# Kernel optimization log

Measured on AMD Instinct MI355X. Metric: run time of the kernel, lower is better.

## Reference

```python
import jax, jax.numpy as jnp
import numpy as np

N = 20000      # nodes
E = 640000     # edges
F = 128        # input features
H = 256        # hidden dim
G = 64         # graphs in batch


def setup_inputs() -> dict:
    key = jax.random.key(0)
    ks = jax.random.split(key, 24)
    w = lambda k, sh: (jax.random.normal(k, sh, jnp.float32) * 0.05)
    inp = {
        'x': jax.random.normal(ks[0], (N, F), jnp.float32),
        'edge_index': jax.random.randint(ks[1], (2, E), 0, N, dtype=jnp.int32),
        'batch': jnp.sort(jax.random.randint(ks[2], (N,), 0, G, dtype=jnp.int32)),
        # GCN stack
        'gcn_w1': w(ks[3], (F, H)), 'gcn_b1': jnp.zeros((H,), jnp.float32),
        'gcn_w2': w(ks[4], (H, H)), 'gcn_b2': jnp.zeros((H,), jnp.float32),
        'gcn_w3': w(ks[5], (H, H)), 'gcn_b3': jnp.zeros((H,), jnp.float32),
        'gcn_w4': w(ks[6], (H, H)), 'gcn_b4': jnp.zeros((H,), jnp.float32),
        # EdgeConv 1: Linear(2F,H) -> ReLU -> Linear(H,H)
        'ec1_w1': w(ks[7], (2 * F, H)), 'ec1_b1': jnp.zeros((H,), jnp.float32),
        'ec1_w2': w(ks[8], (H, H)),     'ec1_b2': jnp.zeros((H,), jnp.float32),
        # EdgeConv 2: Linear(2H,H) -> ReLU -> Linear(H,H)
        'ec2_w1': w(ks[9], (2 * H, H)), 'ec2_b1': jnp.zeros((H,), jnp.float32),
        'ec2_w2': w(ks[10], (H, H)),    'ec2_b2': jnp.zeros((H,), jnp.float32),
        # head
        'fc1_w': w(ks[11], (2 * H, H)), 'fc1_b': jnp.zeros((H,), jnp.float32),
        'out_w': w(ks[12], (H, 1)),     'out_b': jnp.zeros((1,), jnp.float32),
    }
    return inp


def _gcn_conv(x, W, b, src, dst, n):
    # PyG GCNConv: add self loops, symmetric deg^-1/2 normalization, scatter-sum.
    h = x @ W                                        # [n, H]
    loops = jnp.arange(n, dtype=src.dtype)
    s = jnp.concatenate([src, loops])
    d = jnp.concatenate([dst, loops])
    deg = jax.ops.segment_sum(jnp.ones(s.shape[0], x.dtype), d, num_segments=n)
    dinv = jnp.where(deg > 0, jax.lax.rsqrt(deg), 0.0)
    norm = (dinv[s] * dinv[d])[:, None]              # [E+n, 1]
    return jax.ops.segment_sum(h[s] * norm, d, num_segments=n) + b


def _edge_conv(x, w1, b1, w2, b2, src, dst, n):
    # PyG EdgeConv: msg = MLP([x_i, x_j - x_i]), max-aggregate at target i.
    xi = x[dst]
    xj = x[src]
    m = jnp.concatenate([xi, xj - xi], axis=1)       # [E, 2*d]
    m = jax.nn.relu(m @ w1 + b1) @ w2 + b2           # [E, H]
    out = jax.ops.segment_max(m, dst, num_segments=n)
    return jnp.where(jnp.isfinite(out), out, 0.0)    # empty segments -> 0


def reference(x, edge_index, batch,
              gcn_w1, gcn_b1, gcn_w2, gcn_b2, gcn_w3, gcn_b3, gcn_w4, gcn_b4,
              ec1_w1, ec1_b1, ec1_w2, ec1_b2, ec2_w1, ec2_b1, ec2_w2, ec2_b2,
              fc1_w, fc1_b, out_w, out_b):
    n = x.shape[0]
    src, dst = edge_index[0], edge_index[1]
    relu = jax.nn.relu
    # GCN branch (dropout is identity at inference)
    xg = relu(_gcn_conv(x, gcn_w1, gcn_b1, src, dst, n))
    xg = relu(_gcn_conv(xg, gcn_w2, gcn_b2, src, dst, n))
    xg = relu(_gcn_conv(xg, gcn_w3, gcn_b3, src, dst, n))
    xg = relu(_gcn_conv(xg, gcn_w4, gcn_b4, src, dst, n))
    # EdgeConv branch
    xe = relu(_edge_conv(x, ec1_w1, ec1_b1, ec1_w2, ec1_b2, src, dst, n))
    xe = relu(_edge_conv(xe, ec2_w1, ec2_b1, ec2_w2, ec2_b2, src, dst, n))
    # pool per graph + head
    x_cat = jnp.concatenate([xg, xe], axis=1)        # [n, 512]
    g = jax.ops.segment_sum(x_cat, batch, num_segments=G)  # [G, 512]
    g = relu(g @ fc1_w + fc1_b)
    return g @ out_w + out_b                          # [G, 1]
```

## Files before the change

### kernel.cpp

```cpp
#include <hip/hip_runtime.h>

#define HD 256

typedef __attribute__((ext_vector_type(8))) __bf16 bf16x8;
typedef __attribute__((ext_vector_type(4))) __bf16 bf16x4;
typedef __attribute__((ext_vector_type(4))) float f32x4;

static __device__ __forceinline__ float relu_f(float x){ return x > 0.f ? x : 0.f; }

static __device__ __forceinline__ void split4(const float* m, bf16x4& vh, bf16x4& vl){
    #pragma unroll
    for (int j = 0; j < 4; j++){
        float v = m[j];
        __bf16 h = (__bf16)v;
        vh[j] = h;
        vl[j] = (__bf16)(v - (float)h);
    }
}

__global__ void k_count(const int* __restrict__ dst, int* __restrict__ cnt, int E){
    int i = blockIdx.x * blockDim.x + threadIdx.x;
    if (i < E) atomicAdd(&cnt[dst[i]], 1);
}

__global__ void k_dinv(const int* __restrict__ cnt, float* __restrict__ dinv, int n){
    int i = blockIdx.x * blockDim.x + threadIdx.x;
    if (i < n) dinv[i] = 1.0f / sqrtf((float)(cnt[i] + 1));
}

__global__ void k_scan(const int* __restrict__ cnt, int* __restrict__ row_ptr, int n){
    __shared__ int lds[1024];
    int t = threadIdx.x;
    int carry = 0;
    for (int base = 0; base < n; base += 1024){
        int idx = base + t;
        int v = (idx < n) ? cnt[idx] : 0;
        __syncthreads();
        lds[t] = v;
        __syncthreads();
        for (int off = 1; off < 1024; off <<= 1){
            int add = (t >= off) ? lds[t - off] : 0;
            __syncthreads();
            lds[t] += add;
            __syncthreads();
        }
        int incl = lds[t];
        if (idx < n) row_ptr[idx] = carry + incl - v;
        carry += lds[1023];
    }
    if (t == 0) row_ptr[n] = carry;
}

__global__ void k_fill(const int* __restrict__ src, const int* __restrict__ dst,
                       const int* __restrict__ row_ptr, int* __restrict__ fill,
                       int* __restrict__ csr_src, int* __restrict__ csr_dst, int E){
    int i = blockIdx.x * blockDim.x + threadIdx.x;
    if (i < E){
        int d = dst[i];
        int pos = row_ptr[d] + atomicAdd(&fill[d], 1);
        csr_src[pos] = src[i];
        csr_dst[pos] = d;
    }
}

struct PackDesc { const float* src; const float* src2; __bf16* ph; __bf16* pl; int K; int pad; };
struct PackArgs { PackDesc d[10]; };

__global__ void k_wpack_all(PackArgs a){
    PackDesc p = a.d[blockIdx.y];
    int total = (p.K >> 5) * 8192;
    int idx = blockIdx.x * 256 + threadIdx.x;
    if (idx >= total) return;
    int j = idx & 7, g = (idx >> 3) & 3, c = (idx >> 5) & 255, ks = idx >> 13;
    int k = ks * 32 + g * 8 + j;
    float v = p.src[(size_t)k * HD + c];
    if (p.src2) v -= p.src2[(size_t)k * HD + c];
    __bf16 h = (__bf16)v;
    p.ph[idx] = h;
    p.pl[idx] = (__bf16)(v - (float)h);
}

__global__ __launch_bounds__(512, 4) void k_gemm_mfma(
    const float* __restrict__ A,
    const __bf16* __restrict__ Wph, const __bf16* __restrict__ Wpl,
    const float* __restrict__ bias,
    float* __restrict__ C, int M, int K)
{
    __shared__ __bf16 mh[2][64][40];
    __shared__ __bf16 ml[2][64][40];
    int t = threadIdx.x;
    int m0 = blockIdx.x * 64;
    const int w = t >> 6, fr = t & 15, fg = (t & 63) >> 4;
    const int srow = t >> 3, skb = (t & 7) * 4;
    int ar = m0 + srow; if (ar >= M) ar = M - 1;
    const float* Arow = A + (size_t)ar * K + skb;
    const int c0 = w * 32 + fr;
    const int KS = K >> 5;

    f32x4 acc[4][2];
    #pragma unroll
    for (int i = 0; i < 4; i++)
        #pragma unroll
        for (int j = 0; j < 2; j++) acc[i][j] = (f32x4){0.f, 0.f, 0.f, 0.f};

    {
        float4 av = *(const float4*)(Arow);
        float m4[4] = {av.x, av.y, av.z, av.w};
        bf16x4 vh, vl;
        split4(m4, vh, vl);
        *(bf16x4*)&mh[0][srow][skb] = vh;
        *(bf16x4*)&ml[0][srow][skb] = vl;
    }

    for (int ks = 0; ks < KS; ++ks){
        float4 av;
        if (ks + 1 < KS) av = *(const float4*)(Arow + (ks + 1) * 32);
        bf16x8 bh[2], bl[2];
        #pragma unroll
        for (int nf = 0; nf < 2; nf++){
            size_t bi = ((size_t)(ks * 256 + c0 + nf * 16) * 4 + fg) * 8;
            bh[nf] = *(const bf16x8*)(Wph + bi);
            bl[nf] = *(const bf16x8*)(Wpl + bi);
        }
        __syncthreads();
        const int cb = ks & 1;
        #pragma unroll
        for (int mf = 0; mf < 4; mf++){
            bf16x8 ah = *(const bf16x8*)&mh[cb][mf * 16 + fr][fg * 8];
            bf16x8 al = *(const bf16x8*)&ml[cb][mf * 16 + fr][fg * 8];
            #pragma unroll
            for (int nf = 0; nf < 2; nf++){
                acc[mf][nf] = __builtin_amdgcn_mfma_f32_16x16x32_bf16(ah, bh[nf], acc[mf][nf], 0, 0, 0);
                acc[mf][nf] = __builtin_amdgcn_mfma_f32_16x16x32_bf16(al, bh[nf], acc[mf][nf], 0, 0, 0);
                acc[mf][nf] = __builtin_amdgcn_mfma_f32_16x16x32_bf16(ah, bl[nf], acc[mf][nf], 0, 0, 0);
            }
        }
        if (ks + 1 < KS){
            float m4[4] = {av.x, av.y, av.z, av.w};
            bf16x4 vh, vl;
            split4(m4, vh, vl);
            *(bf16x4*)&mh[cb ^ 1][srow][skb] = vh;
            *(bf16x4*)&ml[cb ^ 1][srow][skb] = vl;
        }
    }

    float bj[2];
    #pragma unroll
    for (int nf = 0; nf < 2; nf++) bj[nf] = bias ? bias[c0 + nf * 16] : 0.f;
    #pragma unroll
    for (int mf = 0; mf < 4; mf++)
        #pragma unroll
        for (int reg = 0; reg < 4; reg++){
            int row = m0 + mf * 16 + fg * 4 + reg;
            if (row < M){
                #pragma unroll
                for (int nf = 0; nf < 2; nf++)
                    C[(size_t)row * HD + c0 + nf * 16] = acc[mf][nf][reg] + bj[nf];
            }
        }
}

__global__ __launch_bounds__(256) void k_gcn_agg(const float* __restrict__ h,
                                                 const float* __restrict__ dinv,
                                                 const int* __restrict__ row_ptr,
                                                 const int* __restrict__ csr_src,
                                                 const float* __restrict__ bias,
                                                 float* __restrict__ out, int n){
    int wid = threadIdx.x >> 6, lane = threadIdx.x & 63;
    int i = blockIdx.x * 4 + wid;
    if (i >= n) return;
    float di = dinv[i];
    const float4* hp = (const float4*)h;
    float4 v = hp[(size_t)i * 64 + lane];
    float ax = v.x * di, ay = v.y * di, az = v.z * di, aw = v.w * di;
    int e0 = row_ptr[i], e1 = row_ptr[i + 1];
    for (int e = e0; e < e1; e++){
        int s = csr_src[e];
        float ds = dinv[s];
        float4 u = hp[(size_t)s * 64 + lane];
        ax += u.x * ds; ay += u.y * ds; az += u.z * ds; aw += u.w * ds;
    }
    const float4 b = ((const float4*)bias)[lane];
    float4 o;
    o.x = relu_f(ax * di + b.x);
    o.y = relu_f(ay * di + b.y);
    o.z = relu_f(az * di + b.z);
    o.w = relu_f(aw * di + b.w);
    ((float4*)out)[(size_t)i * 64 + lane] = o;
}

__global__ __launch_bounds__(512, 4) void k_edge_mfma(
    const float* __restrict__ A, const float* __restrict__ B,
    const __bf16* __restrict__ Wph, const __bf16* __restrict__ Wpl,
    const float* __restrict__ bias,
    const int* __restrict__ csr_src, const int* __restrict__ csr_dst,
    float* __restrict__ out, int E)
{
    __shared__ __bf16 mh[2][64][40];
    __shared__ __bf16 ml[2][64][40];
    __shared__ int sdst[64], ssrc[64];
    int t = threadIdx.x;
    int nwg = gridDim.x;
    int q = nwg >> 3, r = nwg & 7;
    int xc = blockIdx.x & 7;
    int bid = (xc < r ? xc * (q + 1) : r * (q + 1) + (xc - r) * q) + (blockIdx.x >> 3);
    int p0 = bid * 64;
    if (t < 64){
        int e = p0 + t; if (e >= E) e = E - 1;
        sdst[t] = csr_dst[e];
        ssrc[t] = csr_src[e];
    }
    __syncthreads();

    const int w  = t >> 6;
    const int fr = t & 15;
    const int fg = (t & 63) >> 4;
    const int srow = t >> 3, skb = (t & 7) * 4;
    const float* Arow = A + (size_t)sdst[srow] * HD + skb;
    const float* Brow = B + (size_t)ssrc[srow] * HD + skb;
    const int c0 = w * 32 + fr;

    f32x4 acc[4][2];
    #pragma unroll
    for (int i = 0; i < 4; i++)
        #pragma unroll
        for (int j = 0; j < 2; j++) acc[i][j] = (f32x4){0.f, 0.f, 0.f, 0.f};

    {
        float4 a = *(const float4*)(Arow);
        float4 g = *(const float4*)(Brow);
        float m4[4] = {relu_f(a.x + g.x), relu_f(a.y + g.y), relu_f(a.z + g.z), relu_f(a.w + g.w)};
        bf16x4 vh, vl;
        split4(m4, vh, vl);
        *(bf16x4*)&mh[0][srow][skb] = vh;
        *(bf16x4*)&ml[0][srow][skb] = vl;
    }

    for (int ks = 0; ks < 8; ++ks){
        float4 a, g;
        if (ks < 7){
            a = *(const float4*)(Arow + (ks + 1) * 32);
            g = *(const float4*)(Brow + (ks + 1) * 32);
        }
        bf16x8 bh[2], bl[2];
        #pragma unroll
        for (int nf = 0; nf < 2; nf++){
            size_t bi = ((size_t)(ks * 256 + c0 + nf * 16) * 4 + fg) * 8;
            bh[nf] = *(const bf16x8*)(Wph + bi);
            bl[nf] = *(const bf16x8*)(Wpl + bi);
        }
        __syncthreads();
        const int cb = ks & 1;
        #pragma unroll
        for (int mf = 0; mf < 4; mf++){
            bf16x8 ah = *(const bf16x8*)&mh[cb][mf * 16 + fr][fg * 8];
            bf16x8 al = *(const bf16x8*)&ml[cb][mf * 16 + fr][fg * 8];
            #pragma unroll
            for (int nf = 0; nf < 2; nf++){
                acc[mf][nf] = __builtin_amdgcn_mfma_f32_16x16x32_bf16(ah, bh[nf], acc[mf][nf], 0, 0, 0);
                acc[mf][nf] = __builtin_amdgcn_mfma_f32_16x16x32_bf16(al, bh[nf], acc[mf][nf], 0, 0, 0);
                acc[mf][nf] = __builtin_amdgcn_mfma_f32_16x16x32_bf16(ah, bl[nf], acc[mf][nf], 0, 0, 0);
            }
        }
        if (ks < 7){
            float m4[4] = {relu_f(a.x + g.x), relu_f(a.y + g.y), relu_f(a.z + g.z), relu_f(a.w + g.w)};
            bf16x4 vh, vl;
            split4(m4, vh, vl);
            *(bf16x4*)&mh[cb ^ 1][srow][skb] = vh;
            *(bf16x4*)&ml[cb ^ 1][srow][skb] = vl;
        }
    }

    float bj[2];
    #pragma unroll
    for (int nf = 0; nf < 2; nf++) bj[nf] = bias[c0 + nf * 16];
    int curd = sdst[fg * 4];
    float v[2];
    #pragma unroll
    for (int nf = 0; nf < 2; nf++) v[nf] = acc[0][nf][0] + bj[nf];
    #pragma unroll
    for (int mf = 0; mf < 4; mf++){
        #pragma unroll
        for (int reg = 0; reg < 4; reg++){
            if (mf == 0 && reg == 0) continue;
            int d = sdst[mf * 16 + fg * 4 + reg];
            if (d != curd){
                #pragma unroll
                for (int nf = 0; nf < 2; nf++)
                    if (v[nf] > 0.f)
                        atomicMax((int*)(out + (size_t)curd * HD + c0 + nf * 16), __float_as_int(v[nf]));
                curd = d;
                #pragma unroll
                for (int nf = 0; nf < 2; nf++) v[nf] = acc[mf][nf][reg] + bj[nf];
            } else {
                #pragma unroll
                for (int nf = 0; nf < 2; nf++) v[nf] = fmaxf(v[nf], acc[mf][nf][reg] + bj[nf]);
            }
        }
    }
    #pragma unroll
    for (int nf = 0; nf < 2; nf++)
        if (v[nf] > 0.f)
            atomicMax((int*)(out + (size_t)curd * HD + c0 + nf * 16), __float_as_int(v[nf]));
}

__global__ __launch_bounds__(512) void k_pool(const float* __restrict__ xg,
                                              const float* __restrict__ xe,
                                              const int* __restrict__ batch,
                                              float* __restrict__ gpool, int n){
    int g = blockIdx.x, t = threadIdx.x;
    int lo, hi;
    { int l = 0, h = n; while (l < h){ int m = (l + h) >> 1; if (batch[m] < g) l = m + 1; else h = m; } lo = l; }
    { int l = lo, h = n; while (l < h){ int m = (l + h) >> 1; if (batch[m] < g + 1) l = m + 1; else h = m; } hi = l; }
    const float* sp = (t < 256) ? (xg + t) : (xe + (t - 256));
    float a0 = 0.f, a1 = 0.f;
    int i = lo;
    for (; i + 1 < hi; i += 2){
        a0 += sp[(size_t)i * HD];
        a1 += sp[(size_t)(i + 1) * HD];
    }
    if (i < hi) a0 += sp[(size_t)i * HD];
    gpool[g * 512 + t] = a0 + a1;
}

__global__ __launch_bounds__(256) void k_head(const float* __restrict__ gpool,
                                              const float* __restrict__ w1,
                                              const float* __restrict__ b1,
                                              const float* __restrict__ w2,
                                              const float* __restrict__ b2,
                                              float* __restrict__ out){
    __shared__ float red[256];
    int g = blockIdx.x, t = threadIdx.x;
    float acc = b1[t];
    const float* gp = gpool + g * 512;
    #pragma unroll 4
    for (int k = 0; k < 512; k++) acc += gp[k] * w1[k * HD + t];
    red[t] = relu_f(acc) * w2[t];
    __syncthreads();
    for (int s = 128; s > 0; s >>= 1){
        if (t < s) red[t] += red[t + s];
        __syncthreads();
    }
    if (t == 0) out[g] = red[0] + b2[0];
}

extern "C" void kernel_launch(void* const* d_in, const int* in_sizes, int n_in,
                              void* d_out, int out_size, void* d_ws, size_t ws_size,
                              hipStream_t stream){
    const float* x      = (const float*)d_in[0];
    const int*   ei     = (const int*)d_in[1];
    const int*   batch  = (const int*)d_in[2];
    const float* gcn_w[4] = {(const float*)d_in[3], (const float*)d_in[5], (const float*)d_in[7], (const float*)d_in[9]};
    const float* gcn_b[4] = {(const float*)d_in[4], (const float*)d_in[6], (const float*)d_in[8], (const float*)d_in[10]};
    const float* ec1_w1 = (const float*)d_in[11]; const float* ec1_b1 = (const float*)d_in[12];
    const float* ec1_w2 = (const float*)d_in[13]; const float* ec1_b2 = (const float*)d_in[14];
    const float* ec2_w1 = (const float*)d_in[15]; const float* ec2_b1 = (const float*)d_in[16];
    const float* ec2_w2 = (const float*)d_in[17]; const float* ec2_b2 = (const float*)d_in[18];
    const float* fc1_w  = (const float*)d_in[19]; const float* fc1_b  = (const float*)d_in[20];
    const float* out_w  = (const float*)d_in[21]; const float* out_b  = (const float*)d_in[22];

    const int N = in_sizes[2];
    const int E = in_sizes[1] / 2;
    const int F = in_sizes[0] / N;
    const int* src = ei;
    const int* dst = ei + E;
    const int GB64 = (N + 63) / 64;
    const int EB   = (E + 63) / 64;

    char* w = (char*)d_ws;
    auto alloc = [&](size_t bytes) -> char* {
        char* p = w;
        w += (bytes + 255) & ~(size_t)255;
        return p;
    };
    int*   cnt     = (int*)alloc((size_t)N * 4);
    int*   fillc   = (int*)alloc((size_t)N * 4);
    int*   row_ptr = (int*)alloc((size_t)(N + 1) * 4);
    int*   csr_src = (int*)alloc((size_t)E * 4);
    int*   csr_dst = (int*)alloc((size_t)E * 4);
    float* dinv    = (float*)alloc((size_t)N * 4);
    float* act     = (float*)alloc((size_t)N * HD * 4);
    float* hbuf    = (float*)alloc((size_t)N * HD * 4);
    float* Bbuf    = (float*)alloc((size_t)N * HD * 4);
    float* xebuf   = (float*)alloc((size_t)N * HD * 4);
    float* gpool   = (float*)alloc((size_t)64 * 512 * 4);
    auto packa = [&](int K) -> __bf16* { return (__bf16*)alloc((size_t)K * 256 * 2); };
    __bf16* pg1h = packa(128); __bf16* pg1l = packa(128);
    __bf16* pg2h = packa(256); __bf16* pg2l = packa(256);
    __bf16* pg3h = packa(256); __bf16* pg3l = packa(256);
    __bf16* pg4h = packa(256); __bf16* pg4l = packa(256);
    __bf16* pe1ah = packa(128); __bf16* pe1al = packa(128);
    __bf16* pe1bh = packa(128); __bf16* pe1bl = packa(128);
    __bf16* pe2ah = packa(256); __bf16* pe2al = packa(256);
    __bf16* pe2bh = packa(256); __bf16* pe2bl = packa(256);
    __bf16* w2h1 = packa(256); __bf16* w2l1 = packa(256);
    __bf16* w2h2 = packa(256); __bf16* w2l2 = packa(256);

    hipMemsetAsync(cnt, 0, (size_t)N * 4, stream);
    hipMemsetAsync(fillc, 0, (size_t)N * 4, stream);
    k_count<<<(E + 255) / 256, 256, 0, stream>>>(dst, cnt, E);
    k_dinv<<<(N + 255) / 256, 256, 0, stream>>>(cnt, dinv, N);
    k_scan<<<1, 1024, 0, stream>>>(cnt, row_ptr, N);
    k_fill<<<(E + 255) / 256, 256, 0, stream>>>(src, dst, row_ptr, fillc, csr_src, csr_dst, E);

    PackArgs pa;
    pa.d[0] = {gcn_w[0],                  nullptr,                    pg1h,  pg1l,  F,  0};
    pa.d[1] = {gcn_w[1],                  nullptr,                    pg2h,  pg2l,  HD, 0};
    pa.d[2] = {gcn_w[2],                  nullptr,                    pg3h,  pg3l,  HD, 0};
    pa.d[3] = {gcn_w[3],                  nullptr,                    pg4h,  pg4l,  HD, 0};
    pa.d[4] = {ec1_w1,                    ec1_w1 + (size_t)F * HD,    pe1ah, pe1al, F,  0};
    pa.d[5] = {ec1_w1 + (size_t)F * HD,   nullptr,                    pe1bh, pe1bl, F,  0};
    pa.d[6] = {ec2_w1,                    ec2_w1 + (size_t)HD * HD,   pe2ah, pe2al, HD, 0};
    pa.d[7] = {ec2_w1 + (size_t)HD * HD,  nullptr,                    pe2bh, pe2bl, HD, 0};
    pa.d[8] = {ec1_w2,                    nullptr,                    w2h1,  w2l1,  HD, 0};
    pa.d[9] = {ec2_w2,                    nullptr,                    w2h2,  w2l2,  HD, 0};
    k_wpack_all<<<dim3(256, 10), 256, 0, stream>>>(pa);

    k_gemm_mfma<<<GB64, 512, 0, stream>>>(x, pg1h, pg1l, nullptr, hbuf, N, F);
    k_gcn_agg<<<(N + 3) / 4, 256, 0, stream>>>(hbuf, dinv, row_ptr, csr_src, gcn_b[0], act, N);
    const __bf16* pgh[3] = {pg2h, pg3h, pg4h};
    const __bf16* pgl[3] = {pg2l, pg3l, pg4l};
    for (int l = 0; l < 3; l++){
        k_gemm_mfma<<<GB64, 512, 0, stream>>>(act, pgh[l], pgl[l], nullptr, hbuf, N, HD);
        k_gcn_agg<<<(N + 3) / 4, 256, 0, stream>>>(hbuf, dinv, row_ptr, csr_src, gcn_b[l + 1], act, N);
    }

    k_gemm_mfma<<<GB64, 512, 0, stream>>>(x, pe1ah, pe1al, ec1_b1, hbuf, N, F);
    k_gemm_mfma<<<GB64, 512, 0, stream>>>(x, pe1bh, pe1bl, nullptr, Bbuf, N, F);
    hipMemsetAsync(xebuf, 0, (size_t)N * HD * 4, stream);
    k_edge_mfma<<<EB, 512, 0, stream>>>(hbuf, Bbuf, w2h1, w2l1, ec1_b2, csr_src, csr_dst, xebuf, E);

    k_gemm_mfma<<<GB64, 512, 0, stream>>>(xebuf, pe2ah, pe2al, ec2_b1, hbuf, N, HD);
    k_gemm_mfma<<<GB64, 512, 0, stream>>>(xebuf, pe2bh, pe2bl, nullptr, Bbuf, N, HD);
    hipMemsetAsync(xebuf, 0, (size_t)N * HD * 4, stream);
    k_edge_mfma<<<EB, 512, 0, stream>>>(hbuf, Bbuf, w2h2, w2l2, ec2_b2, csr_src, csr_dst, xebuf, E);

    k_pool<<<64, 512, 0, stream>>>(act, xebuf, batch, gpool, N);
    k_head<<<64, 256, 0, stream>>>(gpool, fc1_w, fc1_b, out_w, out_b, (float*)d_out);
}
```

Measured before the change: 1.332 ms.

## Prefetch A rows into registers, unroll GCN gather, fuse small kernels

The GEMM is templated on K-steps and now loads all of a thread's A chunks into registers up front. The edge kernel prefetches its gathered rows four steps ahead, hiding global latency behind the MFMA work. The GCN aggregation loop is unrolled by four with independent accumulators so more neighbour gathers are in flight at once. The dinv computation is folded into the scan kernel, and pooling plus the head are fused into one kernel, which removes launches. These changes raise register pressure under the 512x4 launch bounds, and the reordered fp32 sums change rounding slightly.

```diff
diff --git a/kernel.cpp b/kernel.cpp
--- a/kernel.cpp
+++ b/kernel.cpp
@@ -23,18 +23,15 @@
     if (i < E) atomicAdd(&cnt[dst[i]], 1);
 }
 
-__global__ void k_dinv(const int* __restrict__ cnt, float* __restrict__ dinv, int n){
-    int i = blockIdx.x * blockDim.x + threadIdx.x;
-    if (i < n) dinv[i] = 1.0f / sqrtf((float)(cnt[i] + 1));
-}
-
-__global__ void k_scan(const int* __restrict__ cnt, int* __restrict__ row_ptr, int n){
+__global__ void k_scan(const int* __restrict__ cnt, int* __restrict__ row_ptr,
+                       float* __restrict__ dinv, int n){
     __shared__ int lds[1024];
     int t = threadIdx.x;
     int carry = 0;
     for (int base = 0; base < n; base += 1024){
         int idx = base + t;
         int v = (idx < n) ? cnt[idx] : 0;
+        if (idx < n) dinv[idx] = 1.0f / sqrtf((float)(v + 1));
         __syncthreads();
         lds[t] = v;
         __syncthreads();
@@ -80,6 +77,7 @@
     p.pl[idx] = (__bf16)(v - (float)h);
 }
 
+template<int KS>
 __global__ __launch_bounds__(512, 4) void k_gemm_mfma(
     const float* __restrict__ A,
     const __bf16* __restrict__ Wph, const __bf16* __restrict__ Wpl,
@@ -95,26 +93,29 @@
     int ar = m0 + srow; if (ar >= M) ar = M - 1;
     const float* Arow = A + (size_t)ar * K + skb;
     const int c0 = w * 32 + fr;
-    const int KS = K >> 5;
-
-    f32x4 acc[4][2];
-    #pragma unroll
-    for (int i = 0; i < 4; i++)
-        #pragma unroll
-        for (int j = 0; j < 2; j++) acc[i][j] = (f32x4){0.f, 0.f, 0.f, 0.f};
-
-    {
-        float4 av = *(const float4*)(Arow);
-        float m4[4] = {av.x, av.y, av.z, av.w};
+
+    auto stage = [&](int buf, const float4& a){
+        float m4[4] = {a.x, a.y, a.z, a.w};
         bf16x4 vh, vl;
         split4(m4, vh, vl);
-        *(bf16x4*)&mh[0][srow][skb] = vh;
-        *(bf16x4*)&ml[0][srow][skb] = vl;
-    }
-
+        *(bf16x4*)&mh[buf][srow][skb] = vh;
+        *(bf16x4*)&ml[buf][srow][skb] = vl;
+    };
+
+    f32x4 acc[4][2];
+    #pragma unroll
+    for (int i = 0; i < 4; i++)
+        #pragma unroll
+        for (int j = 0; j < 2; j++) acc[i][j] = (f32x4){0.f, 0.f, 0.f, 0.f};
+
+    float4 rA[KS];
+    #pragma unroll
+    for (int c = 0; c < KS; c++) rA[c] = *(const float4*)(Arow + c * 32);
+
+    stage(0, rA[0]);
+
+    #pragma unroll
     for (int ks = 0; ks < KS; ++ks){
-        float4 av;
-        if (ks + 1 < KS) av = *(const float4*)(Arow + (ks + 1) * 32);
         bf16x8 bh[2], bl[2];
         #pragma unroll
         for (int nf = 0; nf < 2; nf++){
@@ -135,13 +136,7 @@
                 acc[mf][nf] = __builtin_amdgcn_mfma_f32_16x16x32_bf16(ah, bl[nf], acc[mf][nf], 0, 0, 0);
             }
         }
-        if (ks + 1 < KS){
-            float m4[4] = {av.x, av.y, av.z, av.w};
-            bf16x4 vh, vl;
-            split4(m4, vh, vl);
-            *(bf16x4*)&mh[cb ^ 1][srow][skb] = vh;
-            *(bf16x4*)&ml[cb ^ 1][srow][skb] = vl;
-        }
+        if (ks + 1 < KS) stage(cb ^ 1, rA[ks + 1]);
     }
 
     float bj[2];
@@ -172,14 +167,34 @@
     float di = dinv[i];
     const float4* hp = (const float4*)h;
     float4 v = hp[(size_t)i * 64 + lane];
-    float ax = v.x * di, ay = v.y * di, az = v.z * di, aw = v.w * di;
+    float ax0 = v.x * di, ay0 = v.y * di, az0 = v.z * di, aw0 = v.w * di;
+    float ax1 = 0.f, ay1 = 0.f, az1 = 0.f, aw1 = 0.f;
+    float ax2 = 0.f, ay2 = 0.f, az2 = 0.f, aw2 = 0.f;
+    float ax3 = 0.f, ay3 = 0.f, az3 = 0.f, aw3 = 0.f;
     int e0 = row_ptr[i], e1 = row_ptr[i + 1];
-    for (int e = e0; e < e1; e++){
+    int e = e0;
+    for (; e + 3 < e1; e += 4){
+        int s0 = csr_src[e], s1 = csr_src[e + 1], s2 = csr_src[e + 2], s3 = csr_src[e + 3];
+        float q0 = dinv[s0], q1 = dinv[s1], q2 = dinv[s2], q3 = dinv[s3];
+        float4 u0 = hp[(size_t)s0 * 64 + lane];
+        float4 u1 = hp[(size_t)s1 * 64 + lane];
+        float4 u2 = hp[(size_t)s2 * 64 + lane];
+        float4 u3 = hp[(size_t)s3 * 64 + lane];
+        ax0 += u0.x * q0; ay0 += u0.y * q0; az0 += u0.z * q0; aw0 += u0.w * q0;
+        ax1 += u1.x * q1; ay1 += u1.y * q1; az1 += u1.z * q1; aw1 += u1.w * q1;
+        ax2 += u2.x * q2; ay2 += u2.y * q2; az2 += u2.z * q2; aw2 += u2.w * q2;
+        ax3 += u3.x * q3; ay3 += u3.y * q3; az3 += u3.z * q3; aw3 += u3.w * q3;
+    }
+    for (; e < e1; e++){
         int s = csr_src[e];
-        float ds = dinv[s];
+        float q = dinv[s];
         float4 u = hp[(size_t)s * 64 + lane];
-        ax += u.x * ds; ay += u.y * ds; az += u.z * ds; aw += u.w * ds;
-    }
+        ax0 += u.x * q; ay0 += u.y * q; az0 += u.z * q; aw0 += u.w * q;
+    }
+    float ax = (ax0 + ax1) + (ax2 + ax3);
+    float ay = (ay0 + ay1) + (ay2 + ay3);
+    float az = (az0 + az1) + (az2 + az3);
+    float aw = (aw0 + aw1) + (aw2 + aw3);
     const float4 b = ((const float4*)bias)[lane];
     float4 o;
     o.x = relu_f(ax * di + b.x);
@@ -220,27 +235,33 @@
     const float* Brow = B + (size_t)ssrc[srow] * HD + skb;
     const int c0 = w * 32 + fr;
 
-    f32x4 acc[4][2];
-    #pragma unroll
-    for (int i = 0; i < 4; i++)
-        #pragma unroll
-        for (int j = 0; j < 2; j++) acc[i][j] = (f32x4){0.f, 0.f, 0.f, 0.f};
-
-    {
-        float4 a = *(const float4*)(Arow);
-        float4 g = *(const float4*)(Brow);
+    auto stage = [&](int buf, const float4& a, const float4& g){
         float m4[4] = {relu_f(a.x + g.x), relu_f(a.y + g.y), relu_f(a.z + g.z), relu_f(a.w + g.w)};
         bf16x4 vh, vl;
         split4(m4, vh, vl);
-        *(bf16x4*)&mh[0][srow][skb] = vh;
-        *(bf16x4*)&ml[0][srow][skb] = vl;
-    }
-
+        *(bf16x4*)&mh[buf][srow][skb] = vh;
+        *(bf16x4*)&ml[buf][srow][skb] = vl;
+    };
+
+    f32x4 acc[4][2];
+    #pragma unroll
+    for (int i = 0; i < 4; i++)
+        #pragma unroll
+        for (int j = 0; j < 2; j++) acc[i][j] = (f32x4){0.f, 0.f, 0.f, 0.f};
+
+    float4 ra[4], rg[4];
+    #pragma unroll
+    for (int c = 0; c < 4; c++){
+        ra[c] = *(const float4*)(Arow + c * 32);
+        rg[c] = *(const float4*)(Brow + c * 32);
+    }
+    stage(0, ra[0], rg[0]);
+
+    #pragma unroll
     for (int ks = 0; ks < 8; ++ks){
-        float4 a, g;
-        if (ks < 7){
-            a = *(const float4*)(Arow + (ks + 1) * 32);
-            g = *(const float4*)(Brow + (ks + 1) * 32);
+        if (ks + 4 < 8){
+            ra[ks & 3] = *(const float4*)(Arow + (ks + 4) * 32);
+            rg[ks & 3] = *(const float4*)(Brow + (ks + 4) * 32);
         }
         bf16x8 bh[2], bl[2];
         #pragma unroll
@@ -262,13 +283,7 @@
                 acc[mf][nf] = __builtin_amdgcn_mfma_f32_16x16x32_bf16(ah, bl[nf], acc[mf][nf], 0, 0, 0);
             }
         }
-        if (ks < 7){
-            float m4[4] = {relu_f(a.x + g.x), relu_f(a.y + g.y), relu_f(a.z + g.z), relu_f(a.w + g.w)};
-            bf16x4 vh, vl;
-            split4(m4, vh, vl);
-            *(bf16x4*)&mh[cb ^ 1][srow][skb] = vh;
-            *(bf16x4*)&ml[cb ^ 1][srow][skb] = vl;
-        }
+        if (ks < 7) stage(cb ^ 1, ra[(ks + 1) & 3], rg[(ks + 1) & 3]);
     }
 
     float bj[2];
@@ -304,10 +319,16 @@
             atomicMax((int*)(out + (size_t)curd * HD + c0 + nf * 16), __float_as_int(v[nf]));
 }
 
-__global__ __launch_bounds__(512) void k_pool(const float* __restrict__ xg,
-                                              const float* __restrict__ xe,
-                                              const int* __restrict__ batch,
-                                              float* __restrict__ gpool, int n){
+__global__ __launch_bounds__(512) void k_pool_head(const float* __restrict__ xg,
+                                                   const float* __restrict__ xe,
+                                                   const int* __restrict__ batch,
+                                                   const float* __restrict__ w1,
+                                                   const float* __restrict__ b1,
+                                                   const float* __restrict__ w2,
+                                                   const float* __restrict__ b2,
+                                                   float* __restrict__ out, int n){
+    __shared__ float gp[512];
+    __shared__ float red[256];
     int g = blockIdx.x, t = threadIdx.x;
     int lo, hi;
     { int l = 0, h = n; while (l < h){ int m = (l + h) >> 1; if (batch[m] < g) l = m + 1; else h = m; } lo = l; }
@@ -320,22 +341,14 @@
         a1 += sp[(size_t)(i + 1) * HD];
     }
     if (i < hi) a0 += sp[(size_t)i * HD];
-    gpool[g * 512 + t] = a0 + a1;
-}
-
-__global__ __launch_bounds__(256) void k_head(const float* __restrict__ gpool,
-                                              const float* __restrict__ w1,
-                                              const float* __restrict__ b1,
-                                              const float* __restrict__ w2,
-                                              const float* __restrict__ b2,
-                                              float* __restrict__ out){
-    __shared__ float red[256];
-    int g = blockIdx.x, t = threadIdx.x;
-    float acc = b1[t];
-    const float* gp = gpool + g * 512;
-    #pragma unroll 4
-    for (int k = 0; k < 512; k++) acc += gp[k] * w1[k * HD + t];
-    red[t] = relu_f(acc) * w2[t];
+    gp[t] = a0 + a1;
+    __syncthreads();
+    if (t < 256){
+        float acc = b1[t];
+        #pragma unroll 4
+        for (int k = 0; k < 512; k++) acc += gp[k] * w1[k * HD + t];
+        red[t] = relu_f(acc) * w2[t];
+    }
     __syncthreads();
     for (int s = 128; s > 0; s >>= 1){
         if (t < s) red[t] += red[t + s];
@@ -383,7 +396,6 @@
     float* hbuf    = (float*)alloc((size_t)N * HD * 4);
     float* Bbuf    = (float*)alloc((size_t)N * HD * 4);
     float* xebuf   = (float*)alloc((size_t)N * HD * 4);
-    float* gpool   = (float*)alloc((size_t)64 * 512 * 4);
     auto packa = [&](int K) -> __bf16* { return (__bf16*)alloc((size_t)K * 256 * 2); };
     __bf16* pg1h = packa(128); __bf16* pg1l = packa(128);
     __bf16* pg2h = packa(256); __bf16* pg2l = packa(256);
@@ -399,8 +411,7 @@
     hipMemsetAsync(cnt, 0, (size_t)N * 4, stream);
     hipMemsetAsync(fillc, 0, (size_t)N * 4, stream);
     k_count<<<(E + 255) / 256, 256, 0, stream>>>(dst, cnt, E);
-    k_dinv<<<(N + 255) / 256, 256, 0, stream>>>(cnt, dinv, N);
-    k_scan<<<1, 1024, 0, stream>>>(cnt, row_ptr, N);
+    k_scan<<<1, 1024, 0, stream>>>(cnt, row_ptr, dinv, N);
     k_fill<<<(E + 255) / 256, 256, 0, stream>>>(src, dst, row_ptr, fillc, csr_src, csr_dst, E);
 
     PackArgs pa;
@@ -416,25 +427,24 @@
     pa.d[9] = {ec2_w2,                    nullptr,                    w2h2,  w2l2,  HD, 0};
     k_wpack_all<<<dim3(256, 10), 256, 0, stream>>>(pa);
 
-    k_gemm_mfma<<<GB64, 512, 0, stream>>>(x, pg1h, pg1l, nullptr, hbuf, N, F);
+    k_gemm_mfma<4><<<GB64, 512, 0, stream>>>(x, pg1h, pg1l, nullptr, hbuf, N, F);
     k_gcn_agg<<<(N + 3) / 4, 256, 0, stream>>>(hbuf, dinv, row_ptr, csr_src, gcn_b[0], act, N);
     const __bf16* pgh[3] = {pg2h, pg3h, pg4h};
     const __bf16* pgl[3] = {pg2l, pg3l, pg4l};
     for (int l = 0; l < 3; l++){
-        k_gemm_mfma<<<GB64, 512, 0, stream>>>(act, pgh[l], pgl[l], nullptr, hbuf, N, HD);
+        k_gemm_mfma<8><<<GB64, 512, 0, stream>>>(act, pgh[l], pgl[l], nullptr, hbuf, N, HD);
         k_gcn_agg<<<(N + 3) / 4, 256, 0, stream>>>(hbuf, dinv, row_ptr, csr_src, gcn_b[l + 1], act, N);
     }
 
-    k_gemm_mfma<<<GB64, 512, 0, stream>>>(x, pe1ah, pe1al, ec1_b1, hbuf, N, F);
-    k_gemm_mfma<<<GB64, 512, 0, stream>>>(x, pe1bh, pe1bl, nullptr, Bbuf, N, F);
+    k_gemm_mfma<4><<<GB64, 512, 0, stream>>>(x, pe1ah, pe1al, ec1_b1, hbuf, N, F);
+    k_gemm_mfma<4><<<GB64, 512, 0, stream>>>(x, pe1bh, pe1bl, nullptr, Bbuf, N, F);
     hipMemsetAsync(xebuf, 0, (size_t)N * HD * 4, stream);
     k_edge_mfma<<<EB, 512, 0, stream>>>(hbuf, Bbuf, w2h1, w2l1, ec1_b2, csr_src, csr_dst, xebuf, E);
 
-    k_gemm_mfma<<<GB64, 512, 0, stream>>>(xebuf, pe2ah, pe2al, ec2_b1, hbuf, N, HD);
-    k_gemm_mfma<<<GB64, 512, 0, stream>>>(xebuf, pe2bh, pe2bl, nullptr, Bbuf, N, HD);
+    k_gemm_mfma<8><<<GB64, 512, 0, stream>>>(xebuf, pe2ah, pe2al, ec2_b1, hbuf, N, HD);
+    k_gemm_mfma<8><<<GB64, 512, 0, stream>>>(xebuf, pe2bh, pe2bl, nullptr, Bbuf, N, HD);
     hipMemsetAsync(xebuf, 0, (size_t)N * HD * 4, stream);
     k_edge_mfma<<<EB, 512, 0, stream>>>(hbuf, Bbuf, w2h2, w2l2, ec2_b2, csr_src, csr_dst, xebuf, E);
 
-    k_pool<<<64, 512, 0, stream>>>(act, xebuf, batch, gpool, N);
-    k_head<<<64, 256, 0, stream>>>(gpool, fc1_w, fc1_b, out_w, out_b, (float*)d_out);
-}
+    k_pool_head<<<64, 512, 0, stream>>>(act, xebuf, batch, fc1_w, fc1_b, out_w, out_b, (float*)d_out, N);
+}
```

After: 1.341 ms. Within noise of the previous version (+0.7%).
